# Optimization experiments

Measured on AMD Instinct MI355X. Metric: run time of the kernel, lower is better.

The kernel has to match this reference:

```python
import jax, jax.numpy as jnp
import numpy as np

POOL = (2, 2)
B, H, W, C = 8, 128, 128, 256
FLAT_OUT = (H * POOL[0]) * (W * POOL[1]) * C  # 16,777,216


def setup_inputs() -> dict:
    key = jax.random.key(0)
    k1, k2 = jax.random.split(key)
    updates = jax.random.normal(k1, (B, H, W, C), dtype=jnp.float32)
    mask = jax.random.randint(k2, (B, H, W, C), 0, FLAT_OUT, dtype=jnp.int32)
    return {"updates": updates, "mask": mask}


def reference(updates, mask):
    ph, pw = POOL
    b, h, w, c = updates.shape
    hout, wout = h * ph, w * pw
    flat_input_size = h * w * c            # NOTE: original uses INPUT size as batch offset
    flat_output_size = hout * wout * c
    # per-batch offset (replicates b * flat_input_size from the TF code)
    batch_range = jnp.arange(b, dtype=jnp.int32).reshape(-1, 1, 1, 1)
    flat_mask = (mask.astype(jnp.int32) + batch_range * flat_input_size).reshape(-1)
    flat_updates = updates.reshape(-1)
    flat_output = jnp.zeros((b * flat_output_size,), dtype=updates.dtype)
    flat_output = flat_output.at[flat_mask].add(flat_updates)
    return flat_output.reshape(b, hout, wout, c)
```

## Files before the change

kernel.cpp:

```cpp
#include <hip/hip_runtime.h>


constexpr int FLAT_IN     = 1 << 22;
constexpr int N_ELEMS     = 8 * FLAT_IN;
constexpr int OUT_WIN     = 7 * FLAT_IN + (1 << 24);
constexpr int OUT_TOTAL   = 134217728;
constexpr int BKT_SHIFT   = 14;
constexpr int BKT_SIZE    = 1 << BKT_SHIFT;
constexpr int NB          = OUT_WIN >> BKT_SHIFT;
constexpr int CHUNK       = 16384;
constexpr int NBLK        = N_ELEMS / CHUNK;
constexpr int SEGS        = 16;
constexpr int SEG_ROWS    = NBLK / SEGS;

constexpr size_t WS_PAIRS  = 0;
constexpr size_t WS_HIST   = 268435456;
constexpr size_t WS_SEGSUM = WS_HIST + (size_t)NBLK * NB * 4;
constexpr size_t WS_BBASE  = WS_SEGSUM + (size_t)SEGS * NB * 4;
constexpr size_t WS_NEEDED = WS_BBASE + (size_t)(NB + 1) * 4;

__global__ __launch_bounds__(256) void zero_kernel(float4* __restrict__ p, int n4) {
  int i = blockIdx.x * 256 + threadIdx.x;
  int stride = gridDim.x * 256;
  for (; i < n4; i += stride) p[i] = make_float4(0.f, 0.f, 0.f, 0.f);
}

__global__ __launch_bounds__(256) void p1_hist(const int4* __restrict__ mask4,
                                               int* __restrict__ hist) {
  __shared__ int cnt[NB];
  const int blk = blockIdx.x, tid = threadIdx.x;
  for (int j = tid; j < NB; j += 256) cnt[j] = 0;
  __syncthreads();
  const int base4 = blk * (CHUNK / 4);
  #pragma unroll
  for (int k = 0; k < CHUNK / 1024; ++k) {
    int j4 = base4 + k * 256 + tid;
    int4 m = mask4[j4];
    int boff = (j4 * 4) & ~(FLAT_IN - 1);
    atomicAdd(&cnt[(m.x + boff) >> BKT_SHIFT], 1);
    atomicAdd(&cnt[(m.y + boff) >> BKT_SHIFT], 1);
    atomicAdd(&cnt[(m.z + boff) >> BKT_SHIFT], 1);
    atomicAdd(&cnt[(m.w + boff) >> BKT_SHIFT], 1);
  }
  __syncthreads();
  for (int j = tid; j < NB; j += 256) hist[blk * NB + j] = cnt[j];
}

__global__ __launch_bounds__(256) void p2_segsum(const int* __restrict__ hist,
                                                 int* __restrict__ segsum) {
  int b = blockIdx.x * 256 + threadIdx.x;
  int seg = blockIdx.y;
  const int* p = hist + (size_t)(seg * SEG_ROWS) * NB + b;
  int s = 0;
  #pragma unroll 4
  for (int k = 0; k < SEG_ROWS; ++k) s += p[(size_t)k * NB];
  segsum[seg * NB + b] = s;
}

__global__ __launch_bounds__(256) void p2_scan(const int* __restrict__ segsum,
                                               int* __restrict__ bbase) {
  __shared__ int tot[NB];
  __shared__ int partial[256];
  const int t = threadIdx.x;
  for (int j = t; j < NB; j += 256) {
    int s = 0;
    #pragma unroll
    for (int g = 0; g < SEGS; ++g) s += segsum[g * NB + j];
    tot[j] = s;
  }
  __syncthreads();
  int local = 0;
  #pragma unroll
  for (int k = 0; k < NB / 256; ++k) local += tot[t * (NB / 256) + k];
  partial[t] = local;
  __syncthreads();
  for (int off = 1; off < 256; off <<= 1) {
    int tmp = (t >= off) ? partial[t - off] : 0;
    __syncthreads();
    partial[t] += tmp;
    __syncthreads();
  }
  int run = partial[t] - local;
  #pragma unroll
  for (int k = 0; k < NB / 256; ++k) {
    int b = t * (NB / 256) + k;
    bbase[b] = run;
    run += tot[b];
  }
  if (t == 255) bbase[NB] = run;
}

__global__ __launch_bounds__(256) void p2_expand(int* __restrict__ hist,
                                                 const int* __restrict__ segsum) {
  int b = blockIdx.x * 256 + threadIdx.x;
  int seg = blockIdx.y;
  int run = 0;
  for (int g = 0; g < seg; ++g) run += segsum[g * NB + b];
  int* p = hist + (size_t)(seg * SEG_ROWS) * NB + b;
  for (int k = 0; k < SEG_ROWS; ++k) {
    int v = p[(size_t)k * NB];
    p[(size_t)k * NB] = run;
    run += v;
  }
}

__global__ __launch_bounds__(256) void p3_place(const int4* __restrict__ mask4,
                                                const float4* __restrict__ upd4,
                                                const int* __restrict__ hist,
                                                const int* __restrict__ bbase,
                                                int2* __restrict__ pairs) {
  __shared__ int cnt[NB];
  __shared__ int rowbase[NB];
  const int blk = blockIdx.x, tid = threadIdx.x;
  for (int j = tid; j < NB; j += 256) {
    cnt[j] = 0;
    rowbase[j] = bbase[j] + hist[blk * NB + j];
  }
  __syncthreads();
  const int base4 = blk * (CHUNK / 4);
  #pragma unroll
  for (int k = 0; k < CHUNK / 1024; ++k) {
    int j4 = base4 + k * 256 + tid;
    int4 m = mask4[j4];
    float4 u = upd4[j4];
    int boff = (j4 * 4) & ~(FLAT_IN - 1);
    {
      int idx = m.x + boff; int b = idx >> BKT_SHIFT;
      int r = atomicAdd(&cnt[b], 1);
      pairs[rowbase[b] + r] = make_int2(idx, __float_as_int(u.x));
    }
    {
      int idx = m.y + boff; int b = idx >> BKT_SHIFT;
      int r = atomicAdd(&cnt[b], 1);
      pairs[rowbase[b] + r] = make_int2(idx, __float_as_int(u.y));
    }
    {
      int idx = m.z + boff; int b = idx >> BKT_SHIFT;
      int r = atomicAdd(&cnt[b], 1);
      pairs[rowbase[b] + r] = make_int2(idx, __float_as_int(u.z));
    }
    {
      int idx = m.w + boff; int b = idx >> BKT_SHIFT;
      int r = atomicAdd(&cnt[b], 1);
      pairs[rowbase[b] + r] = make_int2(idx, __float_as_int(u.w));
    }
  }
}

__global__ __launch_bounds__(256) void p4_apply(const int2* __restrict__ pairs,
                                                const int* __restrict__ bbase,
                                                float* __restrict__ out) {
  __shared__ float win[BKT_SIZE];
  const int bkt = blockIdx.x, tid = threadIdx.x;
  float4* w4 = (float4*)win;
  #pragma unroll
  for (int k = 0; k < BKT_SIZE / 1024; ++k)
    w4[k * 256 + tid] = make_float4(0.f, 0.f, 0.f, 0.f);
  __syncthreads();
  const int s = bbase[bkt], e = bbase[bkt + 1];
  for (int i = s + tid; i < e; i += 256) {
    int2 p = pairs[i];
    atomicAdd(&win[p.x & (BKT_SIZE - 1)], __int_as_float(p.y));
  }
  __syncthreads();
  float4* o4 = (float4*)(out + (size_t)bkt * BKT_SIZE);
  #pragma unroll
  for (int k = 0; k < BKT_SIZE / 1024; ++k)
    o4[k * 256 + tid] = w4[k * 256 + tid];
}

__global__ __launch_bounds__(256) void scatter_add4_kernel(
    const float4* __restrict__ upd4, const int4* __restrict__ msk4,
    float* __restrict__ out, int n4) {
  int j = blockIdx.x * blockDim.x + threadIdx.x;
  if (j >= n4) return;
  float4 u = upd4[j];
  int4 m = msk4[j];
  int base = (j * 4) & ~(FLAT_IN - 1);
  unsafeAtomicAdd(out + (base + m.x), u.x);
  unsafeAtomicAdd(out + (base + m.y), u.y);
  unsafeAtomicAdd(out + (base + m.z), u.z);
  unsafeAtomicAdd(out + (base + m.w), u.w);
}

extern "C" void kernel_launch(void* const* d_in, const int* in_sizes, int n_in,
                              void* d_out, int out_size, void* d_ws, size_t ws_size,
                              hipStream_t stream) {
  const float* updates = (const float*)d_in[0];
  const int*   mask    = (const int*)d_in[1];
  float*       out     = (float*)d_out;
  const int n = in_sizes[0];

  const bool fast = (n == N_ELEMS) && (out_size == OUT_TOTAL) && (ws_size >= WS_NEEDED);

  if (!fast) {
    int n4z = out_size / 4;
    zero_kernel<<<(n4z + 2047) / 2048, 256, 0, stream>>>((float4*)d_out, n4z);
    int n4 = n / 4;
    scatter_add4_kernel<<<(n4 + 255) / 256, 256, 0, stream>>>(
        (const float4*)updates, (const int4*)mask, out, n4);
    return;
  }

  char* ws = (char*)d_ws;
  int2* pairs  = (int2*)(ws + WS_PAIRS);
  int*  hist   = (int*)(ws + WS_HIST);
  int*  segsum = (int*)(ws + WS_SEGSUM);
  int*  bbase  = (int*)(ws + WS_BBASE);

  {
    int n4 = (OUT_TOTAL - OUT_WIN) / 4;
    zero_kernel<<<10752, 256, 0, stream>>>((float4*)(out + OUT_WIN), n4);
  }
  p1_hist<<<NBLK, 256, 0, stream>>>((const int4*)mask, hist);
  p2_segsum<<<dim3(NB / 256, SEGS), 256, 0, stream>>>(hist, segsum);
  p2_scan<<<1, 256, 0, stream>>>(segsum, bbase);
  p2_expand<<<dim3(NB / 256, SEGS), 256, 0, stream>>>(hist, segsum);
  p3_place<<<NBLK, 256, 0, stream>>>((const int4*)mask, (const float4*)updates,
                                     hist, bbase, pairs);
  p4_apply<<<NB, 256, 0, stream>>>(pairs, bbase, out);
}
```

Baseline: 1.300 ms.

## Enlarge bucketing chunks, vectorize pair reads, use nontemporal output stores

Raises the chunk size of the histogram and placement passes to 131072 elements with 1024-thread blocks. This shrinks the per-block histogram matrix and the scan traffic, and the batch offset is hoisted out of the loop. The apply pass now reads two pairs at a time as int4 and handles the odd head and tail separately, and both the zero fill and the final write-out use nontemporal stores. The cost is fewer blocks in p1/p3, which means less parallelism and more shared-atomic contention per block.

```diff
diff --git a/kernel.cpp b/kernel.cpp
--- a/kernel.cpp
+++ b/kernel.cpp
@@ -1,17 +1,21 @@
 #include <hip/hip_runtime.h>
 
 
-constexpr int FLAT_IN     = 1 << 22;
-constexpr int N_ELEMS     = 8 * FLAT_IN;
-constexpr int OUT_WIN     = 7 * FLAT_IN + (1 << 24);
-constexpr int OUT_TOTAL   = 134217728;
-constexpr int BKT_SHIFT   = 14;
-constexpr int BKT_SIZE    = 1 << BKT_SHIFT;
-constexpr int NB          = OUT_WIN >> BKT_SHIFT;
-constexpr int CHUNK       = 16384;
-constexpr int NBLK        = N_ELEMS / CHUNK;
-constexpr int SEGS        = 16;
-constexpr int SEG_ROWS    = NBLK / SEGS;
+typedef float floatx4 __attribute__((ext_vector_type(4)));
+
+constexpr int FLAT_IN   = 1 << 22;
+constexpr int N_ELEMS   = 8 * FLAT_IN;
+constexpr int OUT_WIN   = 7 * FLAT_IN + (1 << 24);
+constexpr int OUT_TOTAL = 134217728;
+constexpr int BKT_SHIFT = 14;
+constexpr int BKT_SIZE  = 1 << BKT_SHIFT;
+constexpr int NB        = OUT_WIN >> BKT_SHIFT;
+constexpr int PBLOCK    = 1024;
+constexpr int CHUNK     = 131072;
+constexpr int NBLK      = N_ELEMS / CHUNK;
+constexpr int ITERS     = CHUNK / (4 * PBLOCK);
+constexpr int SEGS      = 8;
+constexpr int SEG_ROWS  = NBLK / SEGS;
 
 constexpr size_t WS_PAIRS  = 0;
 constexpr size_t WS_HIST   = 268435456;
@@ -19,31 +23,31 @@
 constexpr size_t WS_BBASE  = WS_SEGSUM + (size_t)SEGS * NB * 4;
 constexpr size_t WS_NEEDED = WS_BBASE + (size_t)(NB + 1) * 4;
 
-__global__ __launch_bounds__(256) void zero_kernel(float4* __restrict__ p, int n4) {
+__global__ __launch_bounds__(256) void zero_kernel(floatx4* __restrict__ p, int n4) {
   int i = blockIdx.x * 256 + threadIdx.x;
   int stride = gridDim.x * 256;
-  for (; i < n4; i += stride) p[i] = make_float4(0.f, 0.f, 0.f, 0.f);
-}
-
-__global__ __launch_bounds__(256) void p1_hist(const int4* __restrict__ mask4,
-                                               int* __restrict__ hist) {
+  floatx4 z = {0.f, 0.f, 0.f, 0.f};
+  for (; i < n4; i += stride) __builtin_nontemporal_store(z, p + i);
+}
+
+__global__ __launch_bounds__(PBLOCK) void p1_hist(const int4* __restrict__ mask4,
+                                                  int* __restrict__ hist) {
   __shared__ int cnt[NB];
   const int blk = blockIdx.x, tid = threadIdx.x;
-  for (int j = tid; j < NB; j += 256) cnt[j] = 0;
+  for (int j = tid; j < NB; j += PBLOCK) cnt[j] = 0;
   __syncthreads();
   const int base4 = blk * (CHUNK / 4);
-  #pragma unroll
-  for (int k = 0; k < CHUNK / 1024; ++k) {
-    int j4 = base4 + k * 256 + tid;
-    int4 m = mask4[j4];
-    int boff = (j4 * 4) & ~(FLAT_IN - 1);
+  const int boff = (blk * CHUNK) & ~(FLAT_IN - 1);
+  #pragma unroll 4
+  for (int k = 0; k < ITERS; ++k) {
+    int4 m = mask4[base4 + k * PBLOCK + tid];
     atomicAdd(&cnt[(m.x + boff) >> BKT_SHIFT], 1);
     atomicAdd(&cnt[(m.y + boff) >> BKT_SHIFT], 1);
     atomicAdd(&cnt[(m.z + boff) >> BKT_SHIFT], 1);
     atomicAdd(&cnt[(m.w + boff) >> BKT_SHIFT], 1);
   }
   __syncthreads();
-  for (int j = tid; j < NB; j += 256) hist[blk * NB + j] = cnt[j];
+  for (int j = tid; j < NB; j += PBLOCK) hist[blk * NB + j] = cnt[j];
 }
 
 __global__ __launch_bounds__(256) void p2_segsum(const int* __restrict__ hist,
@@ -104,26 +108,26 @@
   }
 }
 
-__global__ __launch_bounds__(256) void p3_place(const int4* __restrict__ mask4,
-                                                const float4* __restrict__ upd4,
-                                                const int* __restrict__ hist,
-                                                const int* __restrict__ bbase,
-                                                int2* __restrict__ pairs) {
+__global__ __launch_bounds__(PBLOCK) void p3_place(const int4* __restrict__ mask4,
+                                                   const float4* __restrict__ upd4,
+                                                   const int* __restrict__ hist,
+                                                   const int* __restrict__ bbase,
+                                                   int2* __restrict__ pairs) {
   __shared__ int cnt[NB];
   __shared__ int rowbase[NB];
   const int blk = blockIdx.x, tid = threadIdx.x;
-  for (int j = tid; j < NB; j += 256) {
+  for (int j = tid; j < NB; j += PBLOCK) {
     cnt[j] = 0;
     rowbase[j] = bbase[j] + hist[blk * NB + j];
   }
   __syncthreads();
   const int base4 = blk * (CHUNK / 4);
-  #pragma unroll
-  for (int k = 0; k < CHUNK / 1024; ++k) {
-    int j4 = base4 + k * 256 + tid;
+  const int boff = (blk * CHUNK) & ~(FLAT_IN - 1);
+  #pragma unroll 2
+  for (int k = 0; k < ITERS; ++k) {
+    int j4 = base4 + k * PBLOCK + tid;
     int4 m = mask4[j4];
     float4 u = upd4[j4];
-    int boff = (j4 * 4) & ~(FLAT_IN - 1);
     {
       int idx = m.x + boff; int b = idx >> BKT_SHIFT;
       int r = atomicAdd(&cnt[b], 1);
@@ -152,21 +156,33 @@
                                                 float* __restrict__ out) {
   __shared__ float win[BKT_SIZE];
   const int bkt = blockIdx.x, tid = threadIdx.x;
-  float4* w4 = (float4*)win;
+  floatx4* w4 = (floatx4*)win;
+  floatx4 z = {0.f, 0.f, 0.f, 0.f};
+  #pragma unroll
+  for (int k = 0; k < BKT_SIZE / 1024; ++k) w4[k * 256 + tid] = z;
+  __syncthreads();
+  const int s = bbase[bkt], e = bbase[bkt + 1];
+  const int s4 = (s + 1) & ~1;
+  if ((s & 1) && s < e && tid == 0) {
+    int2 p = pairs[s];
+    atomicAdd(&win[p.x & (BKT_SIZE - 1)], __int_as_float(p.y));
+  }
+  const int n2 = (e > s4) ? ((e - s4) >> 1) : 0;
+  const int4* pv = (const int4*)(pairs + s4);
+  for (int i = tid; i < n2; i += 256) {
+    int4 q = pv[i];
+    atomicAdd(&win[q.x & (BKT_SIZE - 1)], __int_as_float(q.y));
+    atomicAdd(&win[q.z & (BKT_SIZE - 1)], __int_as_float(q.w));
+  }
+  if ((e > s4) && ((e - s4) & 1) && tid == 0) {
+    int2 p = pairs[e - 1];
+    atomicAdd(&win[p.x & (BKT_SIZE - 1)], __int_as_float(p.y));
+  }
+  __syncthreads();
+  floatx4* o4 = (floatx4*)(out + (size_t)bkt * BKT_SIZE);
   #pragma unroll
   for (int k = 0; k < BKT_SIZE / 1024; ++k)
-    w4[k * 256 + tid] = make_float4(0.f, 0.f, 0.f, 0.f);
-  __syncthreads();
-  const int s = bbase[bkt], e = bbase[bkt + 1];
-  for (int i = s + tid; i < e; i += 256) {
-    int2 p = pairs[i];
-    atomicAdd(&win[p.x & (BKT_SIZE - 1)], __int_as_float(p.y));
-  }
-  __syncthreads();
-  float4* o4 = (float4*)(out + (size_t)bkt * BKT_SIZE);
-  #pragma unroll
-  for (int k = 0; k < BKT_SIZE / 1024; ++k)
-    o4[k * 256 + tid] = w4[k * 256 + tid];
+    __builtin_nontemporal_store(w4[k * 256 + tid], o4 + k * 256 + tid);
 }
 
 __global__ __launch_bounds__(256) void scatter_add4_kernel(
@@ -195,7 +211,7 @@
 
   if (!fast) {
     int n4z = out_size / 4;
-    zero_kernel<<<(n4z + 2047) / 2048, 256, 0, stream>>>((float4*)d_out, n4z);
+    zero_kernel<<<(n4z + 2047) / 2048, 256, 0, stream>>>((floatx4*)d_out, n4z);
     int n4 = n / 4;
     scatter_add4_kernel<<<(n4 + 255) / 256, 256, 0, stream>>>(
         (const float4*)updates, (const int4*)mask, out, n4);
@@ -210,13 +226,13 @@
 
   {
     int n4 = (OUT_TOTAL - OUT_WIN) / 4;
-    zero_kernel<<<10752, 256, 0, stream>>>((float4*)(out + OUT_WIN), n4);
-  }
-  p1_hist<<<NBLK, 256, 0, stream>>>((const int4*)mask, hist);
+    zero_kernel<<<5376, 256, 0, stream>>>((floatx4*)(out + OUT_WIN), n4);
+  }
+  p1_hist<<<NBLK, PBLOCK, 0, stream>>>((const int4*)mask, hist);
   p2_segsum<<<dim3(NB / 256, SEGS), 256, 0, stream>>>(hist, segsum);
   p2_scan<<<1, 256, 0, stream>>>(segsum, bbase);
   p2_expand<<<dim3(NB / 256, SEGS), 256, 0, stream>>>(hist, segsum);
-  p3_place<<<NBLK, 256, 0, stream>>>((const int4*)mask, (const float4*)updates,
-                                     hist, bbase, pairs);
+  p3_place<<<NBLK, PBLOCK, 0, stream>>>((const int4*)mask, (const float4*)updates,
+                                        hist, bbase, pairs);
   p4_apply<<<NB, 256, 0, stream>>>(pairs, bbase, out);
 }
```

Measured after the change: 1.199 ms. 7.8% less time.
